# Optimization experiments

Hardware: AMD Instinct MI355X
Metric: run time of the kernel (lower is better)

The kernel has to match this reference:

```python
import jax, jax.numpy as jnp
import numpy as np
from jax import lax

N, CIN, COUT = 4, 3, 16
D = H = W = 64
K, S, PAD, OUT_PAD = 3, 2, 1, 1


def setup_inputs() -> dict:
    key = jax.random.key(0)
    k1, k2, k3, k4 = jax.random.split(key, 4)
    x = jax.random.normal(k1, (N, CIN, D, H, W), dtype=jnp.float32)
    # torch ConvTranspose3d weight layout: [Cin, Cout, kD, kH, kW]
    w = jax.random.normal(k2, (CIN, COUT, K, K, K), dtype=jnp.float32) * 0.1
    b = jax.random.normal(k3, (COUT,), dtype=jnp.float32) * 0.1
    subtract = jax.random.normal(k4, (COUT,), dtype=jnp.float32) * 0.1
    return {"x": x, "w": w, "b": b, "subtract": subtract}


def reference(x, w, b, subtract):
    # ConvTranspose3d(k=3, s=2, p=1, output_padding=1) as a dilated conv:
    # flip kernel spatially, swap in/out channel axes, lhs_dilation = stride,
    # padding low = k-1-p = 1, padding high = k-1-p+output_padding = 2.
    w_conv = jnp.flip(jnp.transpose(w, (1, 0, 2, 3, 4)), axis=(2, 3, 4))  # [Cout,Cin,k,k,k]
    y = lax.conv_general_dilated(
        x, w_conv,
        window_strides=(1, 1, 1),
        padding=[(1, 2), (1, 2), (1, 2)],
        lhs_dilation=(S, S, S),
        dimension_numbers=("NCDHW", "OIDHW", "NCDHW"),
    )  # [N, 16, 2D, 2H, 2W]
    y = y + b[None, :, None, None, None]
    # MaxPool3d(kernel=2, stride=2, pad=0)
    y = lax.reduce_window(
        y, -jnp.inf, lax.max,
        window_dimensions=(1, 1, 2, 2, 2),
        window_strides=(1, 1, 2, 2, 2),
        padding="VALID",
    )  # [N, 16, D, H, W]
    s = jax.nn.softmax(y, axis=1)                       # channel softmax
    z = s - subtract[None, :, None, None, None]          # per-channel subtract
    sw = z * jax.nn.sigmoid(z)                           # swish
    return jnp.max(sw, axis=1)                           # max over channels -> [N, D, H, W]
```

## Files before the change

kernel.cpp:

```cpp
#include <hip/hip_runtime.h>
#include <math.h>

#define CIN   3
#define COUT  16
#define DHW   64
#define WPAD  28

typedef float v2f __attribute__((ext_vector_type(2)));

static __device__ __forceinline__ v2f splat2(float s) { v2f r; r.x = s; r.y = s; return r; }

__global__ __launch_bounds__(256, 2) void fused_convt_pool_softmax_swish_max(
    const float* __restrict__ x,
    const float* __restrict__ w,
    const float* __restrict__ bias,
    const float* __restrict__ sub,
    float* __restrict__ out)
{
    __shared__ float wsm[CIN * COUT * WPAD];

    const int tid = threadIdx.y * 32 + threadIdx.x;
    for (int i = tid; i < CIN * COUT * 27; i += 256) {
        const int g = i / 27, r = i - g * 27;
        wsm[g * WPAD + r] = w[i];
    }
    __syncthreads();

    const int tp = threadIdx.x;
    const int h  = blockIdx.x * blockDim.y + threadIdx.y;
    const int d0 = blockIdx.y * 2;
    const int n  = blockIdx.z;
    const int w0 = tp * 2;

    v2f xp[CIN][3][2][2];
    const size_t nbase = (size_t)n * CIN * DHW * DHW * DHW;
    const bool w2ok = (w0 + 2 < DHW);
    const int  off2 = w2ok ? 2 : 0;
#pragma unroll
    for (int c = 0; c < CIN; ++c) {
#pragma unroll
        for (int dd = 0; dd < 3; ++dd) {
#pragma unroll
            for (int hh = 0; hh < 2; ++hh) {
                const int id = d0 + dd;
                const int ih = h + hh;
                float v0 = 0.0f, v1 = 0.0f, v2 = 0.0f;
                if (id < DHW && ih < DHW) {
                    const float* row = x + nbase + (((size_t)c * DHW + id) * DHW + ih) * DHW + w0;
                    const float2 a = *(const float2*)row;
                    v0 = a.x;
                    v1 = a.y;
                    const float t = row[off2];
                    v2 = w2ok ? t : 0.0f;
                }
                v2f p0; p0.x = v0; p0.y = v1;
                v2f p1; p1.x = v1; p1.y = v2;
                xp[c][dd][hh][0] = p0;
                xp[c][dd][hh][1] = p1;
            }
        }
    }

    v2f pooled[2][COUT];
#pragma unroll
    for (int co = 0; co < COUT; ++co) {
        v2f acc[2][2][2][2];
#pragma unroll
        for (int i = 0; i < 16; ++i) (&acc[0][0][0][0])[i] = splat2(0.0f);
#pragma unroll
        for (int c = 0; c < CIN; ++c) {
            const float4* wq = (const float4*)&wsm[(c * COUT + co) * WPAD];
            float4 q[7];
#pragma unroll
            for (int t = 0; t < 7; ++t) q[t] = wq[t];
            const float* wf = (const float*)&q[0];
#pragma unroll
            for (int kd = 0; kd < 3; ++kd) {
                const int pd  = (kd == 1) ? 0 : 1;
                const int dlt = (kd == 0) ? 1 : 0;
#pragma unroll
                for (int kh = 0; kh < 3; ++kh) {
                    const int ph = (kh == 1) ? 0 : 1;
                    const int hh = (kh == 0) ? 1 : 0;
#pragma unroll
                    for (int kw = 0; kw < 3; ++kw) {
                        const int pw = (kw == 1) ? 0 : 1;
                        const int ww = (kw == 0) ? 1 : 0;
                        const v2f wv = splat2(wf[kd * 9 + kh * 3 + kw]);
                        acc[0][pd][ph][pw] = __builtin_elementwise_fma(
                            wv, xp[c][0 + dlt][hh][ww], acc[0][pd][ph][pw]);
                        acc[1][pd][ph][pw] = __builtin_elementwise_fma(
                            wv, xp[c][1 + dlt][hh][ww], acc[1][pd][ph][pw]);
                    }
                }
            }
        }
        const float bco = bias[co];
#pragma unroll
        for (int dout = 0; dout < 2; ++dout) {
            const v2f* a = &acc[dout][0][0][0];
            v2f m0 = __builtin_elementwise_max(__builtin_elementwise_max(a[0], a[1]), a[2]);
            v2f m1 = __builtin_elementwise_max(__builtin_elementwise_max(a[3], a[4]), a[5]);
            v2f m2 = __builtin_elementwise_max(__builtin_elementwise_max(a[6], a[7]), m0);
            pooled[dout][co] = __builtin_elementwise_max(m1, m2) + splat2(bco);
        }
    }

#pragma unroll
    for (int dout = 0; dout < 2; ++dout) {
        v2f m = pooled[dout][0];
#pragma unroll
        for (int co = 1; co < COUT; ++co) m = __builtin_elementwise_max(m, pooled[dout][co]);
        v2f e[COUT];
        v2f s = splat2(0.0f);
#pragma unroll
        for (int co = 0; co < COUT; ++co) {
            v2f t = pooled[dout][co] - m;
            v2f ev; ev.x = __expf(t.x); ev.y = __expf(t.y);
            e[co] = ev;
            s += ev;
        }
        v2f inv; inv.x = __builtin_amdgcn_rcpf(s.x); inv.y = __builtin_amdgcn_rcpf(s.y);
        v2f zmax = splat2(-3.402823466e+38f);
#pragma unroll
        for (int co = 0; co < COUT; ++co)
            zmax = __builtin_elementwise_max(
                zmax, __builtin_elementwise_fma(e[co], inv, splat2(-sub[co])));

        v2f res;
        res.x = zmax.x * __builtin_amdgcn_rcpf(1.0f + __expf(-zmax.x));
        res.y = zmax.y * __builtin_amdgcn_rcpf(1.0f + __expf(-zmax.y));

        float* op = out + (((size_t)n * DHW + (d0 + dout)) * DHW + h) * DHW + w0;
        *(v2f*)op = res;
    }
}

extern "C" void kernel_launch(void* const* d_in, const int* in_sizes, int n_in,
                              void* d_out, int out_size, void* d_ws, size_t ws_size,
                              hipStream_t stream) {
    const float* x   = (const float*)d_in[0];
    const float* w   = (const float*)d_in[1];
    const float* b   = (const float*)d_in[2];
    const float* sub = (const float*)d_in[3];
    float* out = (float*)d_out;

    dim3 block(32, 8, 1);
    dim3 grid(DHW / 8, DHW / 2, 4);
    fused_convt_pool_softmax_swish_max<<<grid, block, 0, stream>>>(x, w, b, sub, out);
}
```

Baseline: 100.5 us.

## Read weights directly from global memory and drop packed v2f math

Removes the shared-memory staging of the weights and the block-wide barrier, so each thread reads weights straight from global memory as wave-uniform addresses that can become scalar loads. It also replaces the packed two-wide float vector FMAs and maxes with scalar float arithmetic and a 3-wide input row instead of duplicated pairs. This cuts LDS traffic, the barrier and register duplication, but gives up packed FMA throughput and depends on the compiler turning the weight reads into scalar loads.

```diff
diff --git a/kernel.cpp b/kernel.cpp
--- a/kernel.cpp
+++ b/kernel.cpp
@@ -4,11 +4,6 @@
 #define CIN   3
 #define COUT  16
 #define DHW   64
-#define WPAD  28
-
-typedef float v2f __attribute__((ext_vector_type(2)));
-
-static __device__ __forceinline__ v2f splat2(float s) { v2f r; r.x = s; r.y = s; return r; }
 
 __global__ __launch_bounds__(256, 2) void fused_convt_pool_softmax_swish_max(
     const float* __restrict__ x,
@@ -17,22 +12,13 @@
     const float* __restrict__ sub,
     float* __restrict__ out)
 {
-    __shared__ float wsm[CIN * COUT * WPAD];
-
-    const int tid = threadIdx.y * 32 + threadIdx.x;
-    for (int i = tid; i < CIN * COUT * 27; i += 256) {
-        const int g = i / 27, r = i - g * 27;
-        wsm[g * WPAD + r] = w[i];
-    }
-    __syncthreads();
-
     const int tp = threadIdx.x;
     const int h  = blockIdx.x * blockDim.y + threadIdx.y;
     const int d0 = blockIdx.y * 2;
     const int n  = blockIdx.z;
     const int w0 = tp * 2;
 
-    v2f xp[CIN][3][2][2];
+    float xr[CIN][3][2][3];
     const size_t nbase = (size_t)n * CIN * DHW * DHW * DHW;
     const bool w2ok = (w0 + 2 < DHW);
     const int  off2 = w2ok ? 2 : 0;
@@ -53,27 +39,22 @@
                     const float t = row[off2];
                     v2 = w2ok ? t : 0.0f;
                 }
-                v2f p0; p0.x = v0; p0.y = v1;
-                v2f p1; p1.x = v1; p1.y = v2;
-                xp[c][dd][hh][0] = p0;
-                xp[c][dd][hh][1] = p1;
+                xr[c][dd][hh][0] = v0;
+                xr[c][dd][hh][1] = v1;
+                xr[c][dd][hh][2] = v2;
             }
         }
     }
 
-    v2f pooled[2][COUT];
+    float pooled[2][2][COUT];
 #pragma unroll
     for (int co = 0; co < COUT; ++co) {
-        v2f acc[2][2][2][2];
+        float acc[2][2][2][2][2];
 #pragma unroll
-        for (int i = 0; i < 16; ++i) (&acc[0][0][0][0])[i] = splat2(0.0f);
+        for (int i = 0; i < 32; ++i) (&acc[0][0][0][0][0])[i] = 0.0f;
 #pragma unroll
         for (int c = 0; c < CIN; ++c) {
-            const float4* wq = (const float4*)&wsm[(c * COUT + co) * WPAD];
-            float4 q[7];
-#pragma unroll
-            for (int t = 0; t < 7; ++t) q[t] = wq[t];
-            const float* wf = (const float*)&q[0];
+            const float* wg = w + ((size_t)c * COUT + co) * 27;
 #pragma unroll
             for (int kd = 0; kd < 3; ++kd) {
                 const int pd  = (kd == 1) ? 0 : 1;
@@ -86,11 +67,14 @@
                     for (int kw = 0; kw < 3; ++kw) {
                         const int pw = (kw == 1) ? 0 : 1;
                         const int ww = (kw == 0) ? 1 : 0;
-                        const v2f wv = splat2(wf[kd * 9 + kh * 3 + kw]);
-                        acc[0][pd][ph][pw] = __builtin_elementwise_fma(
-                            wv, xp[c][0 + dlt][hh][ww], acc[0][pd][ph][pw]);
-                        acc[1][pd][ph][pw] = __builtin_elementwise_fma(
-                            wv, xp[c][1 + dlt][hh][ww], acc[1][pd][ph][pw]);
+                        const float wt = wg[kd * 9 + kh * 3 + kw];
+#pragma unroll
+                        for (int dout = 0; dout < 2; ++dout) {
+                            acc[dout][0][pd][ph][pw] =
+                                fmaf(wt, xr[c][dout + dlt][hh][ww],     acc[dout][0][pd][ph][pw]);
+                            acc[dout][1][pd][ph][pw] =
+                                fmaf(wt, xr[c][dout + dlt][hh][ww + 1], acc[dout][1][pd][ph][pw]);
+                        }
                     }
                 }
             }
@@ -98,41 +82,44 @@
         const float bco = bias[co];
 #pragma unroll
         for (int dout = 0; dout < 2; ++dout) {
-            const v2f* a = &acc[dout][0][0][0];
-            v2f m0 = __builtin_elementwise_max(__builtin_elementwise_max(a[0], a[1]), a[2]);
-            v2f m1 = __builtin_elementwise_max(__builtin_elementwise_max(a[3], a[4]), a[5]);
-            v2f m2 = __builtin_elementwise_max(__builtin_elementwise_max(a[6], a[7]), m0);
-            pooled[dout][co] = __builtin_elementwise_max(m1, m2) + splat2(bco);
+#pragma unroll
+            for (int vx = 0; vx < 2; ++vx) {
+                const float* a = &acc[dout][vx][0][0][0];
+                const float m01 = fmaxf(a[0], a[1]);
+                const float m23 = fmaxf(a[2], a[3]);
+                const float m45 = fmaxf(a[4], a[5]);
+                const float m67 = fmaxf(a[6], a[7]);
+                pooled[dout][vx][co] = fmaxf(fmaxf(m01, m23), fmaxf(m45, m67)) + bco;
+            }
         }
     }
 
 #pragma unroll
     for (int dout = 0; dout < 2; ++dout) {
-        v2f m = pooled[dout][0];
+        float res[2];
 #pragma unroll
-        for (int co = 1; co < COUT; ++co) m = __builtin_elementwise_max(m, pooled[dout][co]);
-        v2f e[COUT];
-        v2f s = splat2(0.0f);
+        for (int vx = 0; vx < 2; ++vx) {
+            float m = pooled[dout][vx][0];
 #pragma unroll
-        for (int co = 0; co < COUT; ++co) {
-            v2f t = pooled[dout][co] - m;
-            v2f ev; ev.x = __expf(t.x); ev.y = __expf(t.y);
-            e[co] = ev;
-            s += ev;
+            for (int co = 1; co < COUT; ++co) m = fmaxf(m, pooled[dout][vx][co]);
+            float e[COUT];
+            float s = 0.0f;
+#pragma unroll
+            for (int co = 0; co < COUT; ++co) {
+                const float ev = __expf(pooled[dout][vx][co] - m);
+                e[co] = ev;
+                s += ev;
+            }
+            const float inv = __builtin_amdgcn_rcpf(s);
+            float zmax = -3.402823466e+38f;
+#pragma unroll
+            for (int co = 0; co < COUT; ++co)
+                zmax = fmaxf(zmax, fmaf(e[co], inv, -sub[co]));
+            res[vx] = zmax * __builtin_amdgcn_rcpf(1.0f + __expf(-zmax));
         }
-        v2f inv; inv.x = __builtin_amdgcn_rcpf(s.x); inv.y = __builtin_amdgcn_rcpf(s.y);
-        v2f zmax = splat2(-3.402823466e+38f);
-#pragma unroll
-        for (int co = 0; co < COUT; ++co)
-            zmax = __builtin_elementwise_max(
-                zmax, __builtin_elementwise_fma(e[co], inv, splat2(-sub[co])));
-
-        v2f res;
-        res.x = zmax.x * __builtin_amdgcn_rcpf(1.0f + __expf(-zmax.x));
-        res.y = zmax.y * __builtin_amdgcn_rcpf(1.0f + __expf(-zmax.y));
-
+        float2 r2; r2.x = res[0]; r2.y = res[1];
         float* op = out + (((size_t)n * DHW + (d0 + dout)) * DHW + h) * DHW + w0;
-        *(v2f*)op = res;
+        *(float2*)op = r2;
     }
 }
 
```

Result: slower. 113.4 us (+12.8%).
